# Optimization experiments

Measured on AMD Instinct MI355X. Metric: run time of the kernel, lower is better.

## Reference

```python
import jax, jax.numpy as jnp
import numpy as np

NEG_SLOPE = 0.2  # PyG GATConv default negative_slope


def gat_conv(x, edge_index, W, att_src, att_dst, bias):
    # PyG GATConv, heads=1, add_self_loops=True, lin bias=False, final bias added
    N = x.shape[0]
    h = x @ W                                     # [N, F]
    loops = jnp.arange(N, dtype=edge_index.dtype)
    src = jnp.concatenate([edge_index[0], loops])
    dst = jnp.concatenate([edge_index[1], loops])
    a_src = h @ att_src                           # [N]
    a_dst = h @ att_dst                           # [N]
    e = a_src[src] + a_dst[dst]
    e = jnp.where(e > 0, e, NEG_SLOPE * e)        # leaky_relu
    m = jax.ops.segment_max(e, dst, num_segments=N)
    w = jnp.exp(e - m[dst])
    denom = jax.ops.segment_sum(w, dst, num_segments=N)
    alpha = w / denom[dst]
    out = jax.ops.segment_sum(h[src] * alpha[:, None], dst, num_segments=N)
    return out + bias


def gcn_conv(x, edge_index, W, b):
    # PyG GCNConv: add self-loops + symmetric normalization
    N = x.shape[0]
    loops = jnp.arange(N, dtype=edge_index.dtype)
    src = jnp.concatenate([edge_index[0], loops])
    dst = jnp.concatenate([edge_index[1], loops])
    deg = jax.ops.segment_sum(jnp.ones(src.shape[0], dtype=x.dtype), dst, num_segments=N)
    dinv = jax.lax.rsqrt(jnp.maximum(deg, 1e-12))  # deg >= 1 thanks to self-loops
    norm = dinv[src] * dinv[dst]
    xw = x @ W
    return jax.ops.segment_sum(xw[src] * norm[:, None], dst, num_segments=N) + b


def get_final_node(x, batch, num_graphs):
    nn_ = jax.ops.segment_sum(jnp.ones(x.shape[0], dtype=jnp.int32), batch, num_segments=num_graphs)
    cum = jnp.concatenate([jnp.zeros(1, dtype=nn_.dtype), jnp.cumsum(nn_)[:-1]])
    return x[cum]


def ontology_emb(table, e1, e2, W, asrc, adst, b, idx_map):
    emb = gat_conv(table, e1, W, asrc, adst, b)
    emb = gat_conv(emb, e2, W, asrc, adst, b)
    return emb[idx_map]


def _forward(spec_emb, diag_table, proce_table, atc_table,
             diag_W, diag_asrc, diag_adst, diag_b,
             proce_W, proce_asrc, proce_adst, proce_b,
             atc_W, atc_asrc, atc_adst, atc_b,
             gcn_W1, gcn_b1, gcn_W2, gcn_b2, gcn_W3, gcn_b3,
             diag_e1, diag_e2, proce_e1, proce_e2, atc_e1, atc_e2,
             diag_map, proce_map, atc_map,
             left_x, left_graph_index, right_x, right_graph_index,
             left_x_batch, right_x_batch, num_graphs):
    diag_emb = ontology_emb(diag_table, diag_e1, diag_e2, diag_W, diag_asrc, diag_adst, diag_b, diag_map)
    proce_emb = ontology_emb(proce_table, proce_e1, proce_e2, proce_W, proce_asrc, proce_adst, proce_b, proce_map)
    atc_emb = ontology_emb(atc_table, atc_e1, atc_e2, atc_W, atc_asrc, atc_adst, atc_b, atc_map)
    all_emb = jnp.concatenate([spec_emb, diag_emb, proce_emb, atc_emb], axis=0)
    lh = all_emb[left_x[:, 0]]   # squeeze(dim=1)
    rh = all_emb[right_x[:, 0]]
    for W, b in ((gcn_W1, gcn_b1), (gcn_W2, gcn_b2), (gcn_W3, gcn_b3)):
        lh = gcn_conv(lh, left_graph_index, W, b)
        rh = gcn_conv(rh, right_graph_index, W, b)
    lf = get_final_node(lh, left_x_batch, num_graphs)
    rf = get_final_node(rh, right_x_batch, num_graphs)
    eps = 1e-6  # CosineSimilarity eps
    num = jnp.sum(lf * rf, axis=-1)
    den = jnp.maximum(jnp.linalg.norm(lf, axis=-1), eps) * jnp.maximum(jnp.linalg.norm(rf, axis=-1), eps)
    return num / den


def setup_inputs() -> dict:
    key = jax.random.key(0)
    ks = jax.random.split(key, 32)
    HID = 128
    B, NPG = 2048, 50
    N = B * NPG               # 102400 nodes per side
    E_PAT = 409600            # 4 edges per node
    DIAG_N, DIAG_L = 30000, 20000
    PROCE_N, PROCE_L = 12000, 8000
    ATC_N, ATC_L = 6000, 4000
    ALL = 1 + DIAG_L + PROCE_L + ATC_L
    f = lambda k, s: jax.random.normal(k, s, dtype=jnp.float32)
    scale = 0.1
    inp = {
        'spec_emb': f(ks[0], (1, HID)),
        'diag_table': f(ks[1], (DIAG_N, HID)),
        'proce_table': f(ks[2], (PROCE_N, HID)),
        'atc_table': f(ks[3], (ATC_N, HID)),
    }
    for i, nm in enumerate(['diag', 'proce', 'atc']):
        inp[nm + '_W'] = f(ks[4 + i], (HID, HID)) * scale
        inp[nm + '_asrc'] = f(ks[7 + i], (HID,)) * scale
        inp[nm + '_adst'] = f(ks[10 + i], (HID,)) * scale
        inp[nm + '_b'] = jnp.zeros((HID,), jnp.float32)
    for j in range(3):
        inp['gcn_W%d' % (j + 1)] = f(ks[13 + j], (HID, HID)) * scale
        inp['gcn_b%d' % (j + 1)] = jnp.zeros((HID,), jnp.float32)
    inp['diag_e1'] = jax.random.randint(ks[16], (2, DIAG_N), 0, DIAG_N, dtype=jnp.int32)
    inp['diag_e2'] = jax.random.randint(ks[17], (2, DIAG_N), 0, DIAG_N, dtype=jnp.int32)
    inp['proce_e1'] = jax.random.randint(ks[18], (2, PROCE_N), 0, PROCE_N, dtype=jnp.int32)
    inp['proce_e2'] = jax.random.randint(ks[19], (2, PROCE_N), 0, PROCE_N, dtype=jnp.int32)
    inp['atc_e1'] = jax.random.randint(ks[20], (2, ATC_N), 0, ATC_N, dtype=jnp.int32)
    inp['atc_e2'] = jax.random.randint(ks[21], (2, ATC_N), 0, ATC_N, dtype=jnp.int32)
    inp['diag_map'] = jnp.arange(DIAG_L, dtype=jnp.int32)
    inp['proce_map'] = jnp.arange(PROCE_L, dtype=jnp.int32)
    inp['atc_map'] = jnp.arange(ATC_L, dtype=jnp.int32)
    inp['left_x'] = jax.random.randint(ks[22], (N, 1), 0, ALL, dtype=jnp.int32)
    inp['right_x'] = jax.random.randint(ks[23], (N, 1), 0, ALL, dtype=jnp.int32)
    inp['left_graph_index'] = jax.random.randint(ks[24], (2, E_PAT), 0, N, dtype=jnp.int32)
    inp['right_graph_index'] = jax.random.randint(ks[25], (2, E_PAT), 0, N, dtype=jnp.int32)
    batch = jnp.repeat(jnp.arange(B, dtype=jnp.int32), NPG)
    inp['left_x_batch'] = batch
    inp['right_x_batch'] = batch
    inp['num_graphs'] = B
    return inp


def reference(spec_emb, diag_table, proce_table, atc_table,
              diag_W, diag_asrc, diag_adst, diag_b,
              proce_W, proce_asrc, proce_adst, proce_b,
              atc_W, atc_asrc, atc_adst, atc_b,
              gcn_W1, gcn_b1, gcn_W2, gcn_b2, gcn_W3, gcn_b3,
              diag_e1, diag_e2, proce_e1, proce_e2, atc_e1, atc_e2,
              diag_map, proce_map, atc_map,
              left_x, left_graph_index, right_x, right_graph_index,
              left_x_batch, right_x_batch, num_graphs):
    return _forward(spec_emb, diag_table, proce_table, atc_table,
                    diag_W, diag_asrc, diag_adst, diag_b,
                    proce_W, proce_asrc, proce_adst, proce_b,
                    atc_W, atc_asrc, atc_adst, atc_b,
                    gcn_W1, gcn_b1, gcn_W2, gcn_b2, gcn_W3, gcn_b3,
                    diag_e1, diag_e2, proce_e1, proce_e2, atc_e1, atc_e2,
                    diag_map, proce_map, atc_map,
                    left_x, left_graph_index, right_x, right_graph_index,
                    left_x_batch, right_x_batch, num_graphs)
```

## Files before the change

kernel.cpp:

```cpp
#include <hip/hip_runtime.h>
#include <hip/hip_bf16.h>

#define HID 128

typedef unsigned int uint;
typedef unsigned short ushort;
typedef short short8 __attribute__((ext_vector_type(8)));
typedef float f32x4 __attribute__((ext_vector_type(4)));

static inline int cdiv_i(long a, long b) { return (int)((a + b - 1) / b); }
static inline int imax_i(int a, int b) { return a > b ? a : b; }

__device__ __forceinline__ float bf2f(uint hi) {
    return __builtin_bit_cast(float, hi << 16);
}
__device__ __forceinline__ ushort f2bf(float f) {
    uint u = __builtin_bit_cast(uint, f);
    u = (u + 0x7fffu + ((u >> 16) & 1u)) >> 16;
    return (ushort)u;
}

struct CsrDesc {
    const int* esrc[8];
    const int* edst[8];
    int ebase[9];
    int nbase[9];
    int totE;
};

template <typename AT>
__device__ __forceinline__ void load_afrag(const AT* __restrict__ A, long row,
                                           int koff, short8& af) {
    if constexpr (__is_same(AT, ushort)) {
        const uint4 raw = *(const uint4*)(A + row * 128 + koff);
        af = __builtin_bit_cast(short8, raw);
    } else {
        const float4* p = (const float4*)(A + row * 128 + koff);
        const float4 x0 = p[0], x1 = p[1];
        af[0] = (short)f2bf(x0.x); af[1] = (short)f2bf(x0.y);
        af[2] = (short)f2bf(x0.z); af[3] = (short)f2bf(x0.w);
        af[4] = (short)f2bf(x1.x); af[5] = (short)f2bf(x1.y);
        af[6] = (short)f2bf(x1.z); af[7] = (short)f2bf(x1.w);
    }
}

struct GOnto {
    const ushort* Wt0; const ushort* Wt1; const ushort* Wt2;
    const float* s0; const float* s1; const float* s2;
    const float* d0; const float* d1; const float* d2;
    int bs1, bs2;
    int r1, r2, r3;
};

template <typename AT>
__device__ void gemm_onto_dev(int b, const AT* __restrict__ x0,
                              const AT* __restrict__ x1, const AT* __restrict__ x2,
                              const GOnto& g, ushort* __restrict__ H,
                              float* __restrict__ as_o, float* __restrict__ ad_o) {
    const int gid = (b >= g.bs1) + (b >= g.bs2);
    const ushort* Wt = (gid == 0) ? g.Wt0 : (gid == 1) ? g.Wt1 : g.Wt2;
    const float* avs = (gid == 0) ? g.s0 : (gid == 1) ? g.s1 : g.s2;
    const float* avd = (gid == 0) ? g.d0 : (gid == 1) ? g.d1 : g.d2;
    const AT* Ag = (gid == 0) ? x0 : (gid == 1) ? x1 : x2;
    const int bloc = b - ((gid == 0) ? 0 : (gid == 1) ? g.bs1 : g.bs2);
    const long rb = (gid == 0) ? 0 : (gid == 1) ? g.r1 : g.r2;
    const long Mg = ((gid == 0) ? g.r1 : (gid == 1) ? g.r2 : g.r3) - rb;

    const int tid = threadIdx.x;
    const int wave = tid >> 6, lane = tid & 63;
    const int r = lane & 15, q = lane >> 4;
    const long m0 = (long)bloc * 128 + wave * 32;

    f32x4 acc[2][8];
#pragma unroll
    for (int mi = 0; mi < 2; ++mi)
#pragma unroll
        for (int ni = 0; ni < 8; ++ni) acc[mi][ni] = (f32x4)0.f;

#pragma unroll
    for (int t = 0; t < 4; ++t) {
        const int koff = t * 32 + q * 8;
        short8 bfr[8];
#pragma unroll
        for (int ni = 0; ni < 8; ++ni) {
            const uint4 raw = *(const uint4*)(Wt + (ni * 16 + r) * 128 + koff);
            bfr[ni] = __builtin_bit_cast(short8, raw);
        }
#pragma unroll
        for (int mi = 0; mi < 2; ++mi) {
            long row = m0 + mi * 16 + r;
            if (row >= Mg) row = Mg - 1;
            short8 af;
            load_afrag<AT>(Ag, row, koff, af);
#pragma unroll
            for (int ni = 0; ni < 8; ++ni)
                acc[mi][ni] = __builtin_amdgcn_mfma_f32_16x16x32_bf16(
                    af, bfr[ni], acc[mi][ni], 0, 0, 0);
        }
    }

    ushort* Hg = H + rb * 128;
#pragma unroll
    for (int mi = 0; mi < 2; ++mi) {
#pragma unroll
        for (int ni = 0; ni < 8; ++ni) {
            const int col = ni * 16 + r;
#pragma unroll
            for (int reg = 0; reg < 4; ++reg) {
                const long row = m0 + mi * 16 + q * 4 + reg;
                if (row < Mg) Hg[row * 128 + col] = f2bf(acc[mi][ni][reg]);
            }
        }
    }

    float asv[8], adv[8];
#pragma unroll
    for (int ni = 0; ni < 8; ++ni) {
        asv[ni] = avs[ni * 16 + r];
        adv[ni] = avd[ni * 16 + r];
    }
#pragma unroll
    for (int mi = 0; mi < 2; ++mi) {
#pragma unroll
        for (int reg = 0; reg < 4; ++reg) {
            float ps = 0.f, pd = 0.f;
#pragma unroll
            for (int ni = 0; ni < 8; ++ni) {
                ps += acc[mi][ni][reg] * asv[ni];
                pd += acc[mi][ni][reg] * adv[ni];
            }
#pragma unroll
            for (int o = 1; o < 16; o <<= 1) {
                ps += __shfl_xor(ps, o);
                pd += __shfl_xor(pd, o);
            }
            const long row = m0 + mi * 16 + q * 4 + reg;
            if (r == 0 && row < Mg) {
                as_o[rb + row] = ps;
                ad_o[rb + row] = pd;
            }
        }
    }
}

__global__ __launch_bounds__(256) void gemm_onto_l2(const ushort* __restrict__ x0,
                                                    const ushort* __restrict__ x1,
                                                    const ushort* __restrict__ x2,
                                                    GOnto g, ushort* __restrict__ H,
                                                    float* __restrict__ as_o,
                                                    float* __restrict__ ad_o) {
    gemm_onto_dev<ushort>(blockIdx.x, x0, x1, x2, g, H, as_o, ad_o);
}

struct EmbSrc {
    const float* spec; const ushort* oE;
    const int* m0; const int* m1; const int* m2;
    int lb2, lb3, r1, r2;
};

__device__ __forceinline__ short8 load_emb(const EmbSrc& e, long row, int koff) {
    short8 af;
    if (row == 0) {
        const float4* pp = (const float4*)(e.spec + koff);
        const float4 x0 = pp[0], x1 = pp[1];
        af[0] = (short)f2bf(x0.x); af[1] = (short)f2bf(x0.y);
        af[2] = (short)f2bf(x0.z); af[3] = (short)f2bf(x0.w);
        af[4] = (short)f2bf(x1.x); af[5] = (short)f2bf(x1.y);
        af[6] = (short)f2bf(x1.z); af[7] = (short)f2bf(x1.w);
        return af;
    }
    const int r = (int)row;
    const int seg = (r >= e.lb2) + (r >= e.lb3);
    const int local = r - ((seg == 0) ? 1 : (seg == 1) ? e.lb2 : e.lb3);
    const int* mp = (seg == 0) ? e.m0 : (seg == 1) ? e.m1 : e.m2;
    const int rb = (seg == 0) ? 0 : (seg == 1) ? e.r1 : e.r2;
    const long sr = (long)rb + mp[local];
    return __builtin_bit_cast(short8, *(const uint4*)(e.oE + sr * 128 + koff));
}

__device__ void gemm_pat_tile(const EmbSrc& es, const ushort* __restrict__ Wt,
                              ushort* __restrict__ C, long m0blk, long rowEnd) {
    const int tid = threadIdx.x;
    const int wave = tid >> 6, lane = tid & 63;
    const int r = lane & 15, q = lane >> 4;
    const long m0 = m0blk + wave * 32;

    f32x4 acc[2][8];
#pragma unroll
    for (int mi = 0; mi < 2; ++mi)
#pragma unroll
        for (int ni = 0; ni < 8; ++ni) acc[mi][ni] = (f32x4)0.f;

#pragma unroll
    for (int t = 0; t < 4; ++t) {
        const int koff = t * 32 + q * 8;
        short8 bfr[8];
#pragma unroll
        for (int ni = 0; ni < 8; ++ni) {
            const uint4 raw = *(const uint4*)(Wt + (ni * 16 + r) * 128 + koff);
            bfr[ni] = __builtin_bit_cast(short8, raw);
        }
#pragma unroll
        for (int mi = 0; mi < 2; ++mi) {
            long row = m0 + mi * 16 + r;
            if (row >= rowEnd) row = rowEnd - 1;
            const short8 af = load_emb(es, row, koff);
#pragma unroll
            for (int ni = 0; ni < 8; ++ni)
                acc[mi][ni] = __builtin_amdgcn_mfma_f32_16x16x32_bf16(
                    af, bfr[ni], acc[mi][ni], 0, 0, 0);
        }
    }

#pragma unroll
    for (int mi = 0; mi < 2; ++mi) {
#pragma unroll
        for (int ni = 0; ni < 8; ++ni) {
            const int col = ni * 16 + r;
#pragma unroll
            for (int reg = 0; reg < 4; ++reg) {
                const long row = m0 + mi * 16 + q * 4 + reg;
                if (row < rowEnd) C[row * 128 + col] = f2bf(acc[mi][ni][reg]);
            }
        }
    }
}

__global__ __launch_bounds__(256) void gemm_pat(EmbSrc es,
                                                const ushort* __restrict__ Wt,
                                                ushort* __restrict__ C, int M) {
    const long m0 = (long)blockIdx.x * 256;
    gemm_pat_tile(es, Wt, C, m0, M);
    if (m0 + 128 < M) gemm_pat_tile(es, Wt, C, m0 + 128, M);
}

__device__ __forceinline__ void fold1_dev(int idx, const float* __restrict__ W2,
                                          const float* __restrict__ b2,
                                          const float* __restrict__ W3,
                                          float* __restrict__ W23b) {
    if (idx >= 129 * 128) return;
    const int i = idx >> 7, j = idx & 127;
    const float* a = (i < 128) ? (W2 + i * 128) : b2;
    float s = 0.f;
#pragma unroll 8
    for (int k = 0; k < 128; ++k) s += a[k] * W3[k * 128 + j];
    W23b[idx] = s;
}

__device__ __forceinline__ void fold2_dev(int idx, const float* __restrict__ W1,
                                          const float* __restrict__ b1,
                                          const float* __restrict__ W23b,
                                          ushort* __restrict__ WpT,
                                          float* __restrict__ cbuf) {
    if (idx >= 130 * 128) return;
    const int i = idx >> 7, j = idx & 127;
    if (i == 129) { cbuf[128 + j] = W23b[128 * 128 + j]; return; }
    const float* a = (i < 128) ? (W1 + i * 128) : b1;
    float s = 0.f;
#pragma unroll 8
    for (int k = 0; k < 128; ++k) s += a[k] * W23b[k * 128 + j];
    if (i < 128) WpT[j * 128 + i] = f2bf(s);
    else cbuf[j] = s;
}

__device__ __forceinline__ void mark_dev(int i, const int* __restrict__ lEg,
                                         const int* __restrict__ rEg, int EP,
                                         int NP, int* __restrict__ mk,
                                         int testBit, int setBit) {
    int src, dst;
    if (i < 2 * EP) {
        const int side = i >= EP;
        const int e = i - side * EP;
        const int* eg = side ? rEg : lEg;
        src = side * NP + eg[e];
        dst = side * NP + eg[EP + e];
    } else if (i < 2 * EP + 2 * NP) {
        src = dst = i - 2 * EP;
    } else return;
    if (mk[dst] & testBit) {
        const int old = mk[src];
        if (!(old & setBit)) mk[src] = old | setBit;
    }
}

__device__ __forceinline__ void csr_count_dev(int i, const CsrDesc& d,
                                              int* __restrict__ cnt) {
    if (i >= d.totE) return;
    int li = 0;
#pragma unroll
    for (int k = 1; k < 8; ++k) li += (i >= d.ebase[k]);
    const int v = d.nbase[li] + d.edst[li][i - d.ebase[li]];
    atomicAdd(&cnt[v], 1);
}

struct PackPrep {
    const float* W2; const float* b2; const float* W3; float* W23b;
    const float* wsrc[3]; ushort* wt_out;
    int* cnt; int NV;
    const int* bL; const int* bR; int NP;
    int* gfL; int* gfR; int* mk;
    int nbF1, nbWT, nbInit;
};

__global__ __launch_bounds__(256) void k_prep(PackPrep p) {
    const int b = blockIdx.x, tid = threadIdx.x;
    if (b < p.nbF1) {
        fold1_dev(b * 256 + tid, p.W2, p.b2, p.W3, p.W23b);
    } else if (b < p.nbF1 + p.nbWT) {
        const int idx = (b - p.nbF1) * 256 + tid;
        if (idx < 3 * 16384) {
            const int m = idx >> 14;
            const int e = idx & 16383;
            const int n = e >> 7, k = e & 127;
            p.wt_out[idx] = f2bf(p.wsrc[m][k * 128 + n]);
        }
    } else {
        const int i = (b - p.nbF1 - p.nbWT) * 256 + tid;
        if (i < p.NV) p.cnt[i] = 0;
        if (i < 2 * p.NP) {
            const int side = i >= p.NP;
            const int ii = i - (side ? p.NP : 0);
            const int* bb = side ? p.bR : p.bL;
            int* gf = side ? p.gfR : p.gfL;
            const int cur = bb[ii];
            const int prev = (ii == 0) ? -1 : bb[ii - 1];
            int m = 0;
            if (cur > prev) {
                for (int g = prev + 1; g <= cur; ++g) gf[g] = ii;
                m = 1;
            }
            p.mk[i] = m;
        }
    }
}

struct PackBig {
    const float* x0; const float* x1; const float* x2;
    GOnto go; ushort* H; float* as_o; float* ad_o;
    const float* W1; const float* b1; const float* W23b;
    ushort* WpT; float* cbuf;
    CsrDesc dsc; int* cnt;
    const int* lEg; const int* rEg; int EP; int NP; int* mk;
    int nbGemm, nbF2, nbCnt;
};

__global__ __launch_bounds__(256) void k_big1(PackBig p) {
    const int b = blockIdx.x, tid = threadIdx.x;
    if (b < p.nbGemm) {
        gemm_onto_dev<float>(b, p.x0, p.x1, p.x2, p.go, p.H, p.as_o, p.ad_o);
    } else if (b < p.nbGemm + p.nbF2) {
        fold2_dev((b - p.nbGemm) * 256 + tid, p.W1, p.b1, p.W23b, p.WpT, p.cbuf);
    } else if (b < p.nbGemm + p.nbF2 + p.nbCnt) {
        csr_count_dev((b - p.nbGemm - p.nbF2) * 256 + tid, p.dsc, p.cnt);
    } else {
        mark_dev((b - p.nbGemm - p.nbF2 - p.nbCnt) * 256 + tid, p.lEg, p.rEg,
                 p.EP, p.NP, p.mk, 1, 2);
    }
}

__device__ void scan_tile_dev(const int* __restrict__ in, int* __restrict__ out,
                              int* __restrict__ bsum, int n, int pn0, int pcnt,
                              float* __restrict__ dinv, int tb, int tid,
                              int* sbuf) {
    const int base = tb * 1024 + tid * 4;
    int v[4];
    int s = 0;
#pragma unroll
    for (int k = 0; k < 4; ++k) {
        const int i = base + k;
        v[k] = (i < n) ? (in[i] + 1) : 0;
        if (i >= pn0 && i < pn0 + pcnt)
            dinv[i - pn0] = rsqrtf(fmaxf((float)v[k], 1e-12f));
        s += v[k];
    }
    sbuf[tid] = s;
    __syncthreads();
    int x = s;
    for (int o = 1; o < 256; o <<= 1) {
        const int t = (tid >= o) ? sbuf[tid - o] : 0;
        __syncthreads();
        x += t;
        sbuf[tid] = x;
        __syncthreads();
    }
    int run = x - s;
#pragma unroll
    for (int k = 0; k < 4; ++k) {
        const int i = base + k;
        if (i < n) out[i] = run;
        run += v[k];
    }
    if (tid == 255) bsum[tb] = x;
}

struct PackScan {
    const int* cnt; int* offs; int* bsum;
    int NV; int pn0; int pcnt; float* dinv;
    const int* lEg; const int* rEg; int EP; int NP; int* mk;
    int nbScan;
};

__global__ __launch_bounds__(256) void k_scan(PackScan p) {
    __shared__ int sbuf[256];
    const int b = blockIdx.x, tid = threadIdx.x;
    if (b < p.nbScan) {
        scan_tile_dev(p.cnt, p.offs, p.bsum, p.NV, p.pn0, p.pcnt, p.dinv, b,
                      tid, sbuf);
    } else {
        mark_dev((b - p.nbScan) * 256 + tid, p.lEg, p.rEg, p.EP, p.NP, p.mk,
                 2, 4);
    }
}

__global__ __launch_bounds__(256) void k_scanfin(int* __restrict__ out,
                                                 int* __restrict__ out2,
                                                 const int* __restrict__ bsum,
                                                 int n, int nbData) {
    __shared__ int sbuf[256];
    const int tb = blockIdx.x, tid = threadIdx.x;
    int pLim = tb < nbData ? tb : nbData;
    int pth = 0;
    for (int j = tid; j < pLim; j += 256) pth += bsum[j];
    sbuf[tid] = pth;
    __syncthreads();
    for (int o = 128; o > 0; o >>= 1) {
        if (tid < o) sbuf[tid] += sbuf[tid + o];
        __syncthreads();
    }
    const int prefix = sbuf[0];
    const int base = tb * 1024 + tid * 4;
#pragma unroll
    for (int k = 0; k < 4; ++k) {
        const int i = base + k;
        if (i < n) {
            const int v = out[i] + prefix;
            out[i] = v;
            out2[i] = v;
        } else if (i == n) {
            out[i] = prefix + ((tb < nbData) ? bsum[tb] : 0);
        }
    }
}

struct FillP {
    CsrDesc dsc;
    const int* offs; int* offs2; const int* cnt;
    int* srcl; int4* pedge; const float* dinv;
    const int* lx; const int* rx; const int* mk;
    int NP, pB;
    int eStart, eCount, vStart, vCount;
};

__device__ void fill_dev(const FillP& f, int idx) {
    if (idx < f.eCount) {
        const int i = f.eStart + idx;
        int li = 0;
#pragma unroll
        for (int k = 1; k < 8; ++k) li += (i >= f.dsc.ebase[k]);
        const int j = i - f.dsc.ebase[li];
        const int v = f.dsc.nbase[li] + f.dsc.edst[li][j];
        const int s = f.dsc.esrc[li][j];
        if (li >= 6) {
            const int n2l = v - f.dsc.nbase[6];
            if (f.mk[n2l] == 0) return;
            const int sg = (li - 6) * f.NP + s;
            const int cidx = atomicAdd(&f.offs2[v], 1);
            int4 rec;
            rec.x = sg;
            rec.y = (li == 7 ? f.rx : f.lx)[s];
            rec.z = __float_as_int(f.dinv[n2l] * f.dinv[sg]);
            rec.w = 0;
            f.pedge[cidx - f.pB] = rec;
        } else {
            const int cidx = atomicAdd(&f.offs2[v], 1);
            f.srcl[cidx] = s;
        }
    } else if (idx < f.eCount + f.vCount) {
        const int v = f.vStart + (idx - f.eCount);
        int li = 0;
#pragma unroll
        for (int k = 1; k < 8; ++k) li += (v >= f.dsc.nbase[k]);
        const int s = v - f.dsc.nbase[li];
        if (li >= 6) {
            const int n2l = v - f.dsc.nbase[6];
            if (f.mk[n2l] == 0) return;
            const int cidx = f.offs[v] + f.cnt[v];
            const int sg = (li - 6) * f.NP + s;
            int4 rec;
            rec.x = sg;
            rec.y = (li == 7 ? f.rx : f.lx)[s];
            rec.z = __float_as_int(f.dinv[n2l] * f.dinv[sg]);
            rec.w = 0;
            f.pedge[cidx - f.pB] = rec;
        } else {
            f.srcl[f.offs[v] + f.cnt[v]] = s;
        }
    }
}

__global__ __launch_bounds__(256) void k_fill(FillP f) {
    fill_dev(f, blockIdx.x * 256 + threadIdx.x);
}

struct GatP {
    int r1, r2;
    int ob0, ob1, ob2;
    const float* b0; const float* b1; const float* b2;
};

__device__ __forceinline__ void acc8(float* acc, float w, const uint4 v) {
    acc[0] += w * bf2f(v.x & 0xffff);
    acc[1] += w * bf2f(v.x >> 16);
    acc[2] += w * bf2f(v.y & 0xffff);
    acc[3] += w * bf2f(v.y >> 16);
    acc[4] += w * bf2f(v.z & 0xffff);
    acc[5] += w * bf2f(v.z >> 16);
    acc[6] += w * bf2f(v.w & 0xffff);
    acc[7] += w * bf2f(v.w >> 16);
}

__device__ void gat_dev(int node, int ql, const ushort* __restrict__ h,
                        const float* __restrict__ as, const float* __restrict__ ad,
                        const int* __restrict__ offs, const int* __restrict__ srcl,
                        const GatP& p, ushort* __restrict__ out, int Mtot) {
    if (node >= Mtot) return;
    const int gid = (node >= p.r1) + (node >= p.r2);
    const int rb = (gid == 0) ? 0 : (gid == 1) ? p.r1 : p.r2;
    const int ob = (gid == 0) ? p.ob0 : (gid == 1) ? p.ob1 : p.ob2;
    const float* bias = (gid == 0) ? p.b0 : (gid == 1) ? p.b1 : p.b2;
    const int local = node - rb;
    const int beg = offs[ob + local], end = offs[ob + local + 1];
    const float adv = ad[node];
    float denom = 0.f;
    float acc[8] = {0.f, 0.f, 0.f, 0.f, 0.f, 0.f, 0.f, 0.f};
    int j = beg;
    for (; j + 2 <= end; j += 2) {
        const int s0 = srcl[j], s1 = srcl[j + 1];
        float e0 = as[rb + s0] + adv; e0 = (e0 > 0.f) ? e0 : 0.2f * e0;
        float e1 = as[rb + s1] + adv; e1 = (e1 > 0.f) ? e1 : 0.2f * e1;
        const float w0 = __expf(e0), w1 = __expf(e1);
        const uint4 v0 = *(const uint4*)(h + (size_t)(rb + s0) * 128 + ql * 8);
        const uint4 v1 = *(const uint4*)(h + (size_t)(rb + s1) * 128 + ql * 8);
        denom += w0 + w1;
        acc8(acc, w0, v0);
        acc8(acc, w1, v1);
    }
    if (j < end) {
        const int s0 = srcl[j];
        float e0 = as[rb + s0] + adv; e0 = (e0 > 0.f) ? e0 : 0.2f * e0;
        const float w0 = __expf(e0);
        const uint4 v0 = *(const uint4*)(h + (size_t)(rb + s0) * 128 + ql * 8);
        denom += w0;
        acc8(acc, w0, v0);
    }
    const float inv = 1.f / denom;
    const float4 bv0 = *(const float4*)(bias + ql * 8);
    const float4 bv1 = *(const float4*)(bias + ql * 8 + 4);
    uint4 o;
    o.x = (uint)f2bf(acc[0] * inv + bv0.x) | ((uint)f2bf(acc[1] * inv + bv0.y) << 16);
    o.y = (uint)f2bf(acc[2] * inv + bv0.z) | ((uint)f2bf(acc[3] * inv + bv0.w) << 16);
    o.z = (uint)f2bf(acc[4] * inv + bv1.x) | ((uint)f2bf(acc[5] * inv + bv1.y) << 16);
    o.w = (uint)f2bf(acc[6] * inv + bv1.z) | ((uint)f2bf(acc[7] * inv + bv1.w) << 16);
    *(uint4*)(out + (size_t)node * 128 + ql * 8) = o;
}

__global__ __launch_bounds__(256) void gat_all(const ushort* __restrict__ h,
                                               const float* __restrict__ as,
                                               const float* __restrict__ ad,
                                               const int* __restrict__ offs,
                                               const int* __restrict__ srcl,
                                               GatP p, ushort* __restrict__ out,
                                               int Mtot) {
    gat_dev(blockIdx.x * 16 + (threadIdx.x >> 4), threadIdx.x & 15, h, as, ad,
            offs, srcl, p, out, Mtot);
}

struct GatFill {
    const ushort* h; const float* as; const float* ad;
    const int* offs; const int* srcl;
    GatP gp; ushort* out; int Mtot; int nbGat;
    FillP f;
};

__global__ __launch_bounds__(256) void k_gat_fill(GatFill g) {
    const int b = blockIdx.x, tid = threadIdx.x;
    if (b < g.nbGat) {
        gat_dev(b * 16 + (tid >> 4), tid & 15, g.h, g.as, g.ad, g.offs, g.srcl,
                g.gp, g.out, g.Mtot);
    } else {
        fill_dev(g.f, (b - g.nbGat) * 256 + tid);
    }
}

__global__ __launch_bounds__(256) void gcn_agg1(const ushort* __restrict__ A3,
                                                const int4* __restrict__ pedge,
                                                const int* __restrict__ offs6,
                                                const float* __restrict__ c1,
                                                ushort* __restrict__ t1,
                                                const int* __restrict__ mk,
                                                int NP2, int pB) {
    const int n2 = blockIdx.x * 16 + (threadIdx.x >> 4);
    const int ql = threadIdx.x & 15;
    if (n2 >= NP2) return;
    if ((mk[n2] & 4) == 0) return;
    const int beg = offs6[n2] - pB, end = offs6[n2 + 1] - pB;
    float acc[8] = {0.f, 0.f, 0.f, 0.f, 0.f, 0.f, 0.f, 0.f};
    int j = beg;
    for (; j + 2 <= end; j += 2) {
        const int4 r0 = pedge[j], r1 = pedge[j + 1];
        const float w0 = __int_as_float(r0.z), w1 = __int_as_float(r1.z);
        const uint4 v0 = *(const uint4*)(A3 + (size_t)r0.y * 128 + ql * 8);
        const uint4 v1 = *(const uint4*)(A3 + (size_t)r1.y * 128 + ql * 8);
        acc8(acc, w0, v0);
        acc8(acc, w1, v1);
    }
    if (j < end) {
        const int4 r0 = pedge[j];
        const uint4 v0 = *(const uint4*)(A3 + (size_t)r0.y * 128 + ql * 8);
        acc8(acc, __int_as_float(r0.z), v0);
    }
    const float4 bv0 = *(const float4*)(c1 + ql * 8);
    const float4 bv1 = *(const float4*)(c1 + ql * 8 + 4);
    uint4 o;
    o.x = (uint)f2bf(acc[0] + bv0.x) | ((uint)f2bf(acc[1] + bv0.y) << 16);
    o.y = (uint)f2bf(acc[2] + bv0.z) | ((uint)f2bf(acc[3] + bv0.w) << 16);
    o.z = (uint)f2bf(acc[4] + bv1.x) | ((uint)f2bf(acc[5] + bv1.y) << 16);
    o.w = (uint)f2bf(acc[6] + bv1.z) | ((uint)f2bf(acc[7] + bv1.w) << 16);
    *(uint4*)(t1 + (size_t)n2 * 128 + ql * 8) = o;
}

__device__ __forceinline__ void gcn_q_acc(const ushort* __restrict__ x,
                                          const int4* __restrict__ pedge,
                                          int beg, int end, int ql, float* acc) {
    int j = beg;
    for (; j + 2 <= end; j += 2) {
        const int4 r0 = pedge[j], r1 = pedge[j + 1];
        const float w0 = __int_as_float(r0.z), w1 = __int_as_float(r1.z);
        const uint4 v0 = *(const uint4*)(x + (size_t)r0.x * 128 + ql * 8);
        const uint4 v1 = *(const uint4*)(x + (size_t)r1.x * 128 + ql * 8);
        acc8(acc, w0, v0);
        acc8(acc, w1, v1);
    }
    if (j < end) {
        const int4 r0 = pedge[j];
        const uint4 v0 = *(const uint4*)(x + (size_t)r0.x * 128 + ql * 8);
        acc8(acc, __int_as_float(r0.z), v0);
    }
}

__global__ __launch_bounds__(256) void gcn_agg2(const ushort* __restrict__ t1,
                                                const int4* __restrict__ pedge,
                                                const int* __restrict__ offs6,
                                                const float* __restrict__ c2,
                                                ushort* __restrict__ t2,
                                                const int* __restrict__ mk,
                                                int NP2, int pB) {
    const int n2 = blockIdx.x * 16 + (threadIdx.x >> 4);
    const int ql = threadIdx.x & 15;
    if (n2 >= NP2) return;
    if ((mk[n2] & 2) == 0) return;
    const int beg = offs6[n2] - pB, end = offs6[n2 + 1] - pB;
    float acc[8] = {0.f, 0.f, 0.f, 0.f, 0.f, 0.f, 0.f, 0.f};
    gcn_q_acc(t1, pedge, beg, end, ql, acc);
    const float4 bv0 = *(const float4*)(c2 + ql * 8);
    const float4 bv1 = *(const float4*)(c2 + ql * 8 + 4);
    uint4 o;
    o.x = (uint)f2bf(acc[0] + bv0.x) | ((uint)f2bf(acc[1] + bv0.y) << 16);
    o.y = (uint)f2bf(acc[2] + bv0.z) | ((uint)f2bf(acc[3] + bv0.w) << 16);
    o.z = (uint)f2bf(acc[4] + bv1.x) | ((uint)f2bf(acc[5] + bv1.y) << 16);
    o.w = (uint)f2bf(acc[6] + bv1.z) | ((uint)f2bf(acc[7] + bv1.w) << 16);
    *(uint4*)(t2 + (size_t)n2 * 128 + ql * 8) = o;
}

__global__ __launch_bounds__(256) void final_cos(const ushort* __restrict__ t2,
                                                 const int4* __restrict__ pedge,
                                                 const int* __restrict__ offs6,
                                                 const int* __restrict__ gfL,
                                                 const int* __restrict__ gfR,
                                                 const float* __restrict__ b3,
                                                 float* __restrict__ out,
                                                 int B, int NP, int pB) {
    const int g = blockIdx.x * 8 + (threadIdx.x >> 5);
    const int l32 = threadIdx.x & 31;
    const int side = l32 >> 4;
    const int ql = l32 & 15;
    if (g >= B) return;
    const int n2 = (side ? NP : 0) + (side ? gfR : gfL)[g];
    const int beg = offs6[n2] - pB, end = offs6[n2 + 1] - pB;
    float acc[8] = {0.f, 0.f, 0.f, 0.f, 0.f, 0.f, 0.f, 0.f};
    gcn_q_acc(t2, pedge, beg, end, ql, acc);
    const float4 bv0 = *(const float4*)(b3 + ql * 8);
    const float4 bv1 = *(const float4*)(b3 + ql * 8 + 4);
    float v[8];
    v[0] = acc[0] + bv0.x; v[1] = acc[1] + bv0.y;
    v[2] = acc[2] + bv0.z; v[3] = acc[3] + bv0.w;
    v[4] = acc[4] + bv1.x; v[5] = acc[5] + bv1.y;
    v[6] = acc[6] + bv1.z; v[7] = acc[7] + bv1.w;
    float num = 0.f, nself = 0.f, nother = 0.f;
#pragma unroll
    for (int j = 0; j < 8; ++j) {
        const float o = __shfl_xor(v[j], 16);
        num += v[j] * o;
        nself += v[j] * v[j];
        nother += o * o;
    }
#pragma unroll
    for (int o1 = 1; o1 < 16; o1 <<= 1) {
        num += __shfl_xor(num, o1);
        nself += __shfl_xor(nself, o1);
        nother += __shfl_xor(nother, o1);
    }
    if (l32 == 0)
        out[g] = num / (fmaxf(sqrtf(nself), 1e-6f) * fmaxf(sqrtf(nother), 1e-6f));
}

extern "C" void kernel_launch(void* const* d_in, const int* in_sizes, int n_in,
                              void* d_out, int out_size, void* d_ws, size_t ws_size,
                              hipStream_t stream) {
    (void)n_in; (void)ws_size;
    const float* spec = (const float*)d_in[0];
    const float* tabs[3] = {(const float*)d_in[1], (const float*)d_in[2], (const float*)d_in[3]};
    const float* ontW[3] = {(const float*)d_in[4], (const float*)d_in[8], (const float*)d_in[12]};
    const float* ontAs[3] = {(const float*)d_in[5], (const float*)d_in[9], (const float*)d_in[13]};
    const float* ontAd[3] = {(const float*)d_in[6], (const float*)d_in[10], (const float*)d_in[14]};
    const float* ontB[3] = {(const float*)d_in[7], (const float*)d_in[11], (const float*)d_in[15]};
    const float* gcnW[3] = {(const float*)d_in[16], (const float*)d_in[18], (const float*)d_in[20]};
    const float* gcnB[3] = {(const float*)d_in[17], (const float*)d_in[19], (const float*)d_in[21]};
    const int* e1s[3] = {(const int*)d_in[22], (const int*)d_in[24], (const int*)d_in[26]};
    const int* e2s[3] = {(const int*)d_in[23], (const int*)d_in[25], (const int*)d_in[27]};
    const int* maps[3] = {(const int*)d_in[28], (const int*)d_in[29], (const int*)d_in[30]};
    const int* left_x = (const int*)d_in[31];
    const int* right_x = (const int*)d_in[32];
    const int* left_eg = (const int*)d_in[33];
    const int* right_eg = (const int*)d_in[34];
    const int* left_batch = (const int*)d_in[35];
    const int* right_batch = (const int*)d_in[36];

    int Ms[3] = {in_sizes[1] / HID, in_sizes[2] / HID, in_sizes[3] / HID};
    int E1s[3] = {in_sizes[22] / 2, in_sizes[24] / 2, in_sizes[26] / 2};
    int E2s[3] = {in_sizes[23] / 2, in_sizes[25] / 2, in_sizes[27] / 2};
    int Ls[3] = {in_sizes[28], in_sizes[29], in_sizes[30]};
    const int NP = in_sizes[31];
    const int EP = in_sizes[33] / 2;
    const int B = out_size;
    const long ALL = 1 + (long)Ls[0] + Ls[1] + Ls[2];
    const int Mtot = Ms[0] + Ms[1] + Ms[2];
    const int r1 = Ms[0], r2 = Ms[0] + Ms[1];

    CsrDesc dsc;
    int eCnt[8], nCnt[8];
    for (int i = 0; i < 3; ++i) {
        dsc.esrc[i] = e1s[i];     dsc.edst[i] = e1s[i] + E1s[i];
        eCnt[i] = E1s[i];         nCnt[i] = Ms[i];
        dsc.esrc[3 + i] = e2s[i]; dsc.edst[3 + i] = e2s[i] + E2s[i];
        eCnt[3 + i] = E2s[i];     nCnt[3 + i] = Ms[i];
    }
    dsc.esrc[6] = left_eg;  dsc.edst[6] = left_eg + EP;  eCnt[6] = EP; nCnt[6] = NP;
    dsc.esrc[7] = right_eg; dsc.edst[7] = right_eg + EP; eCnt[7] = EP; nCnt[7] = NP;
    dsc.ebase[0] = 0;
    int nb_acc = 0;
    for (int i = 0; i < 8; ++i) {
        dsc.ebase[i + 1] = dsc.ebase[i] + eCnt[i];
        dsc.nbase[i] = nb_acc;
        nb_acc += nCnt[i];
    }
    const int NV = nb_acc;
    dsc.nbase[8] = NV;
    dsc.totE = dsc.ebase[8];
    const int totEntries = dsc.totE + NV;
    const int pB = dsc.ebase[6] + dsc.nbase[6];
    const int pEntries = totEntries - pB;

    char* ws = (char*)d_ws;
    size_t off = 0;
    auto alloc = [&](size_t bytes) -> void* {
        off = (off + 255) & ~(size_t)255;
        void* p = ws + off;
        off += bytes;
        return p;
    };
    ushort* wt4 = (ushort*)alloc((size_t)4 * 16384 * 2);
    float* W23b = (float*)alloc((size_t)129 * 128 * 4);
    float* cbuf = (float*)alloc((size_t)256 * 4);
    ushort* A3 = (ushort*)alloc((size_t)ALL * HID * 2);
    int* cnt = (int*)alloc((size_t)NV * 4);
    int* offs = (int*)alloc((size_t)(NV + 1) * 4);
    int* offs2 = (int*)alloc((size_t)NV * 4);
    int* srcl = (int*)alloc((size_t)pB * 4);
    int4* pedge = (int4*)alloc((size_t)pEntries * 16);
    int* bsum = (int*)alloc(1025 * 4);
    float* dinv = (float*)alloc((size_t)2 * NP * 4);
    float* as = (float*)alloc((size_t)Mtot * 4);
    float* ad = (float*)alloc((size_t)Mtot * 4);
    int* gfL = (int*)alloc((size_t)(B + 1) * 4);
    int* gfR = (int*)alloc((size_t)(B + 1) * 4);
    int* mk = (int*)alloc((size_t)2 * NP * 4);
    ushort* t1 = (ushort*)alloc((size_t)2 * NP * HID * 2);
    ushort* big = (ushort*)alloc((size_t)2 * NP * HID * 2);
    ushort* hbuf = big;
    ushort* obuf = big + (size_t)Mtot * HID;
    ushort* t2 = big;

    const ushort* wtOnt[3] = {wt4, wt4 + 16384, wt4 + 2 * 16384};
    ushort* WpT = wt4 + 3 * 16384;
    const float* c1 = cbuf;
    const float* c2 = cbuf + 128;

    PackPrep pp;
    pp.W2 = gcnW[1]; pp.b2 = gcnB[1]; pp.W3 = gcnW[2]; pp.W23b = W23b;
    pp.wsrc[0] = ontW[0]; pp.wsrc[1] = ontW[1]; pp.wsrc[2] = ontW[2];
    pp.wt_out = wt4;
    pp.cnt = cnt; pp.NV = NV;
    pp.bL = left_batch; pp.bR = right_batch; pp.NP = NP;
    pp.gfL = gfL; pp.gfR = gfR; pp.mk = mk;
    pp.nbF1 = cdiv_i(129 * 128, 256);
    pp.nbWT = cdiv_i(3 * 16384, 256);
    pp.nbInit = cdiv_i(imax_i(NV, 2 * NP), 256);
    k_prep<<<pp.nbF1 + pp.nbWT + pp.nbInit, 256, 0, stream>>>(pp);

    GOnto go;
    go.Wt0 = wtOnt[0]; go.Wt1 = wtOnt[1]; go.Wt2 = wtOnt[2];
    go.s0 = ontAs[0]; go.s1 = ontAs[1]; go.s2 = ontAs[2];
    go.d0 = ontAd[0]; go.d1 = ontAd[1]; go.d2 = ontAd[2];
    go.bs1 = cdiv_i(Ms[0], 128);
    go.bs2 = go.bs1 + cdiv_i(Ms[1], 128);
    const int totBlk = go.bs2 + cdiv_i(Ms[2], 128);
    go.r1 = r1; go.r2 = r2; go.r3 = Mtot;

    PackBig pg;
    pg.x0 = tabs[0]; pg.x1 = tabs[1]; pg.x2 = tabs[2];
    pg.go = go; pg.H = hbuf; pg.as_o = as; pg.ad_o = ad;
    pg.W1 = gcnW[0]; pg.b1 = gcnB[0]; pg.W23b = W23b;
    pg.WpT = WpT; pg.cbuf = cbuf;
    pg.dsc = dsc; pg.cnt = cnt;
    pg.lEg = left_eg; pg.rEg = right_eg; pg.EP = EP; pg.NP = NP; pg.mk = mk;
    pg.nbGemm = totBlk;
    pg.nbF2 = cdiv_i(130 * 128, 256);
    pg.nbCnt = cdiv_i(dsc.totE, 256);
    const int nbMark = cdiv_i(2 * EP + 2 * NP, 256);
    k_big1<<<pg.nbGemm + pg.nbF2 + pg.nbCnt + nbMark, 256, 0, stream>>>(pg);

    PackScan psn;
    psn.cnt = cnt; psn.offs = offs; psn.bsum = bsum;
    psn.NV = NV; psn.pn0 = dsc.nbase[6]; psn.pcnt = 2 * NP; psn.dinv = dinv;
    psn.lEg = left_eg; psn.rEg = right_eg; psn.EP = EP; psn.NP = NP; psn.mk = mk;
    psn.nbScan = cdiv_i(NV, 1024);
    k_scan<<<psn.nbScan + nbMark, 256, 0, stream>>>(psn);

    k_scanfin<<<cdiv_i(NV + 1, 1024), 256, 0, stream>>>(offs, offs2, bsum, NV,
                                                        psn.nbScan);

    FillP fb;
    fb.dsc = dsc; fb.offs = offs; fb.offs2 = offs2; fb.cnt = cnt;
    fb.srcl = srcl; fb.pedge = pedge; fb.dinv = dinv;
    fb.lx = left_x; fb.rx = right_x; fb.mk = mk;
    fb.NP = NP; fb.pB = pB;

    FillP fo = fb;
    fo.eStart = 0;             fo.eCount = dsc.ebase[3];
    fo.vStart = 0;             fo.vCount = dsc.nbase[3];
    k_fill<<<cdiv_i(fo.eCount + fo.vCount, 256), 256, 0, stream>>>(fo);

    GatFill gf;
    gf.h = hbuf; gf.as = as; gf.ad = ad; gf.offs = offs; gf.srcl = srcl;
    gf.gp = GatP{r1, r2, dsc.nbase[0], dsc.nbase[1], dsc.nbase[2],
                 ontB[0], ontB[1], ontB[2]};
    gf.out = obuf; gf.Mtot = Mtot;
    gf.nbGat = cdiv_i(Mtot, 16);
    gf.f = fb;
    gf.f.eStart = dsc.ebase[3]; gf.f.eCount = dsc.totE - dsc.ebase[3];
    gf.f.vStart = dsc.nbase[3]; gf.f.vCount = NV - dsc.nbase[3];
    k_gat_fill<<<gf.nbGat + cdiv_i(gf.f.eCount + gf.f.vCount, 256), 256, 0,
                 stream>>>(gf);

    gemm_onto_l2<<<totBlk, 256, 0, stream>>>(obuf, obuf + (size_t)r1 * HID,
                                             obuf + (size_t)r2 * HID, go, hbuf,
                                             as, ad);
    const GatP gp1{r1, r2, dsc.nbase[3], dsc.nbase[4], dsc.nbase[5],
                   ontB[0], ontB[1], ontB[2]};
    gat_all<<<cdiv_i(Mtot, 16), 256, 0, stream>>>(hbuf, as, ad, offs, srcl, gp1,
                                                  obuf, Mtot);

    EmbSrc es;
    es.spec = spec; es.oE = obuf;
    es.m0 = maps[0]; es.m1 = maps[1]; es.m2 = maps[2];
    es.lb2 = 1 + Ls[0]; es.lb3 = 1 + Ls[0] + Ls[1];
    es.r1 = r1; es.r2 = r2;
    gemm_pat<<<cdiv_i(ALL, 256), 256, 0, stream>>>(es, WpT, A3, (int)ALL);

    const int* offs6 = offs + dsc.nbase[6];
    gcn_agg1<<<cdiv_i(2 * NP, 16), 256, 0, stream>>>(A3, pedge, offs6, c1, t1,
                                                     mk, 2 * NP, pB);
    gcn_agg2<<<cdiv_i(2 * NP, 16), 256, 0, stream>>>(t1, pedge, offs6, c2, t2,
                                                     mk, 2 * NP, pB);
    final_cos<<<cdiv_i(B, 8), 256, 0, stream>>>(t2, pedge, offs6, gfL, gfR,
                                                gcnB[2], (float*)d_out, B, NP, pB);
}
```

Measured before the change: 334.3 us.

## Pack CSR degree counters into bytes and shrink GEMM tiles to 64 rows

Replaces the per-node int degree counters with 8-bit fields packed four to a uint. Counting uses shifted atomicAdds and the scan and fill kernels read the counters through byte extraction. This shrinks the counter memory and lets the scan read one word per thread, but it assumes no in-degree exceeds 255. Separately, the ontology and pattern GEMMs now use 64-row blocks with one 16-row MFMA tile per wave, giving more blocks and fewer registers but re-reading the B fragments more often.

```diff
diff --git a/kernel.cpp b/kernel.cpp
--- a/kernel.cpp
+++ b/kernel.cpp
@@ -18,6 +18,10 @@
     uint u = __builtin_bit_cast(uint, f);
     u = (u + 0x7fffu + ((u >> 16) & 1u)) >> 16;
     return (ushort)u;
+}
+
+__device__ __forceinline__ int cnt_rd(const uint* __restrict__ cnt, int v) {
+    return (int)((cnt[v >> 2] >> ((v & 3) * 8)) & 0xffu);
 }
 
 struct CsrDesc {
@@ -69,13 +73,11 @@
     const int tid = threadIdx.x;
     const int wave = tid >> 6, lane = tid & 63;
     const int r = lane & 15, q = lane >> 4;
-    const long m0 = (long)bloc * 128 + wave * 32;
-
-    f32x4 acc[2][8];
-#pragma unroll
-    for (int mi = 0; mi < 2; ++mi)
-#pragma unroll
-        for (int ni = 0; ni < 8; ++ni) acc[mi][ni] = (f32x4)0.f;
+    const long m0 = (long)bloc * 64 + wave * 16;
+
+    f32x4 acc[8];
+#pragma unroll
+    for (int ni = 0; ni < 8; ++ni) acc[ni] = (f32x4)0.f;
 
 #pragma unroll
     for (int t = 0; t < 4; ++t) {
@@ -86,30 +88,24 @@
             const uint4 raw = *(const uint4*)(Wt + (ni * 16 + r) * 128 + koff);
             bfr[ni] = __builtin_bit_cast(short8, raw);
         }
-#pragma unroll
-        for (int mi = 0; mi < 2; ++mi) {
-            long row = m0 + mi * 16 + r;
-            if (row >= Mg) row = Mg - 1;
-            short8 af;
-            load_afrag<AT>(Ag, row, koff, af);
-#pragma unroll
-            for (int ni = 0; ni < 8; ++ni)
-                acc[mi][ni] = __builtin_amdgcn_mfma_f32_16x16x32_bf16(
-                    af, bfr[ni], acc[mi][ni], 0, 0, 0);
-        }
+        long row = m0 + r;
+        if (row >= Mg) row = Mg - 1;
+        short8 af;
+        load_afrag<AT>(Ag, row, koff, af);
+#pragma unroll
+        for (int ni = 0; ni < 8; ++ni)
+            acc[ni] = __builtin_amdgcn_mfma_f32_16x16x32_bf16(af, bfr[ni],
+                                                              acc[ni], 0, 0, 0);
     }
 
     ushort* Hg = H + rb * 128;
 #pragma unroll
-    for (int mi = 0; mi < 2; ++mi) {
-#pragma unroll
-        for (int ni = 0; ni < 8; ++ni) {
-            const int col = ni * 16 + r;
-#pragma unroll
-            for (int reg = 0; reg < 4; ++reg) {
-                const long row = m0 + mi * 16 + q * 4 + reg;
-                if (row < Mg) Hg[row * 128 + col] = f2bf(acc[mi][ni][reg]);
-            }
+    for (int ni = 0; ni < 8; ++ni) {
+        const int col = ni * 16 + r;
+#pragma unroll
+        for (int reg = 0; reg < 4; ++reg) {
+            const long row = m0 + q * 4 + reg;
+            if (row < Mg) Hg[row * 128 + col] = f2bf(acc[ni][reg]);
         }
     }
 
@@ -120,25 +116,22 @@
         adv[ni] = avd[ni * 16 + r];
     }
 #pragma unroll
-    for (int mi = 0; mi < 2; ++mi) {
-#pragma unroll
-        for (int reg = 0; reg < 4; ++reg) {
-            float ps = 0.f, pd = 0.f;
-#pragma unroll
-            for (int ni = 0; ni < 8; ++ni) {
-                ps += acc[mi][ni][reg] * asv[ni];
-                pd += acc[mi][ni][reg] * adv[ni];
-            }
-#pragma unroll
-            for (int o = 1; o < 16; o <<= 1) {
-                ps += __shfl_xor(ps, o);
-                pd += __shfl_xor(pd, o);
-            }
-            const long row = m0 + mi * 16 + q * 4 + reg;
-            if (r == 0 && row < Mg) {
-                as_o[rb + row] = ps;
-                ad_o[rb + row] = pd;
-            }
+    for (int reg = 0; reg < 4; ++reg) {
+        float ps = 0.f, pd = 0.f;
+#pragma unroll
+        for (int ni = 0; ni < 8; ++ni) {
+            ps += acc[ni][reg] * asv[ni];
+            pd += acc[ni][reg] * adv[ni];
+        }
+#pragma unroll
+        for (int o = 1; o < 16; o <<= 1) {
+            ps += __shfl_xor(ps, o);
+            pd += __shfl_xor(pd, o);
+        }
+        const long row = m0 + q * 4 + reg;
+        if (r == 0 && row < Mg) {
+            as_o[rb + row] = ps;
+            ad_o[rb + row] = pd;
         }
     }
 }
@@ -178,18 +171,17 @@
     return __builtin_bit_cast(short8, *(const uint4*)(e.oE + sr * 128 + koff));
 }
 
-__device__ void gemm_pat_tile(const EmbSrc& es, const ushort* __restrict__ Wt,
-                              ushort* __restrict__ C, long m0blk, long rowEnd) {
+__global__ __launch_bounds__(256) void gemm_pat(EmbSrc es,
+                                                const ushort* __restrict__ Wt,
+                                                ushort* __restrict__ C, int M) {
     const int tid = threadIdx.x;
     const int wave = tid >> 6, lane = tid & 63;
     const int r = lane & 15, q = lane >> 4;
-    const long m0 = m0blk + wave * 32;
-
-    f32x4 acc[2][8];
-#pragma unroll
-    for (int mi = 0; mi < 2; ++mi)
-#pragma unroll
-        for (int ni = 0; ni < 8; ++ni) acc[mi][ni] = (f32x4)0.f;
+    const long m0 = (long)blockIdx.x * 64 + wave * 16;
+
+    f32x4 acc[8];
+#pragma unroll
+    for (int ni = 0; ni < 8; ++ni) acc[ni] = (f32x4)0.f;
 
 #pragma unroll
     for (int t = 0; t < 4; ++t) {
@@ -200,38 +192,24 @@
             const uint4 raw = *(const uint4*)(Wt + (ni * 16 + r) * 128 + koff);
             bfr[ni] = __builtin_bit_cast(short8, raw);
         }
-#pragma unroll
-        for (int mi = 0; mi < 2; ++mi) {
-            long row = m0 + mi * 16 + r;
-            if (row >= rowEnd) row = rowEnd - 1;
-            const short8 af = load_emb(es, row, koff);
-#pragma unroll
-            for (int ni = 0; ni < 8; ++ni)
-                acc[mi][ni] = __builtin_amdgcn_mfma_f32_16x16x32_bf16(
-                    af, bfr[ni], acc[mi][ni], 0, 0, 0);
-        }
-    }
-
-#pragma unroll
-    for (int mi = 0; mi < 2; ++mi) {
-#pragma unroll
-        for (int ni = 0; ni < 8; ++ni) {
-            const int col = ni * 16 + r;
-#pragma unroll
-            for (int reg = 0; reg < 4; ++reg) {
-                const long row = m0 + mi * 16 + q * 4 + reg;
-                if (row < rowEnd) C[row * 128 + col] = f2bf(acc[mi][ni][reg]);
-            }
-        }
-    }
-}
-
-__global__ __launch_bounds__(256) void gemm_pat(EmbSrc es,
-                                                const ushort* __restrict__ Wt,
-                                                ushort* __restrict__ C, int M) {
-    const long m0 = (long)blockIdx.x * 256;
-    gemm_pat_tile(es, Wt, C, m0, M);
-    if (m0 + 128 < M) gemm_pat_tile(es, Wt, C, m0 + 128, M);
+        long row = m0 + r;
+        if (row >= M) row = M - 1;
+        const short8 af = load_emb(es, row, koff);
+#pragma unroll
+        for (int ni = 0; ni < 8; ++ni)
+            acc[ni] = __builtin_amdgcn_mfma_f32_16x16x32_bf16(af, bfr[ni],
+                                                              acc[ni], 0, 0, 0);
+    }
+
+#pragma unroll
+    for (int ni = 0; ni < 8; ++ni) {
+        const int col = ni * 16 + r;
+#pragma unroll
+        for (int reg = 0; reg < 4; ++reg) {
+            const long row = m0 + q * 4 + reg;
+            if (row < M) C[row * 128 + col] = f2bf(acc[ni][reg]);
+        }
+    }
 }
 
 __device__ __forceinline__ void fold1_dev(int idx, const float* __restrict__ W2,
@@ -284,19 +262,19 @@
 }
 
 __device__ __forceinline__ void csr_count_dev(int i, const CsrDesc& d,
-                                              int* __restrict__ cnt) {
+                                              uint* __restrict__ cnt) {
     if (i >= d.totE) return;
     int li = 0;
 #pragma unroll
     for (int k = 1; k < 8; ++k) li += (i >= d.ebase[k]);
     const int v = d.nbase[li] + d.edst[li][i - d.ebase[li]];
-    atomicAdd(&cnt[v], 1);
+    atomicAdd(&cnt[v >> 2], 1u << ((v & 3) * 8));
 }
 
 struct PackPrep {
     const float* W2; const float* b2; const float* W3; float* W23b;
     const float* wsrc[3]; ushort* wt_out;
-    int* cnt; int NV;
+    uint* cnt; int cntW;
     const int* bL; const int* bR; int NP;
     int* gfL; int* gfR; int* mk;
     int nbF1, nbWT, nbInit;
@@ -316,7 +294,7 @@
         }
     } else {
         const int i = (b - p.nbF1 - p.nbWT) * 256 + tid;
-        if (i < p.NV) p.cnt[i] = 0;
+        if (i < p.cntW) p.cnt[i] = 0;
         if (i < 2 * p.NP) {
             const int side = i >= p.NP;
             const int ii = i - (side ? p.NP : 0);
@@ -339,7 +317,7 @@
     GOnto go; ushort* H; float* as_o; float* ad_o;
     const float* W1; const float* b1; const float* W23b;
     ushort* WpT; float* cbuf;
-    CsrDesc dsc; int* cnt;
+    CsrDesc dsc; uint* cnt;
     const int* lEg; const int* rEg; int EP; int NP; int* mk;
     int nbGemm, nbF2, nbCnt;
 };
@@ -358,17 +336,18 @@
     }
 }
 
-__device__ void scan_tile_dev(const int* __restrict__ in, int* __restrict__ out,
+__device__ void scan_tile_dev(const uint* __restrict__ in, int* __restrict__ out,
                               int* __restrict__ bsum, int n, int pn0, int pcnt,
                               float* __restrict__ dinv, int tb, int tid,
                               int* sbuf) {
     const int base = tb * 1024 + tid * 4;
+    const uint word = in[tb * 256 + tid];
     int v[4];
     int s = 0;
 #pragma unroll
     for (int k = 0; k < 4; ++k) {
         const int i = base + k;
-        v[k] = (i < n) ? (in[i] + 1) : 0;
+        v[k] = (i < n) ? (int)((word >> (k * 8)) & 0xffu) + 1 : 0;
         if (i >= pn0 && i < pn0 + pcnt)
             dinv[i - pn0] = rsqrtf(fmaxf((float)v[k], 1e-12f));
         s += v[k];
@@ -394,7 +373,7 @@
 }
 
 struct PackScan {
-    const int* cnt; int* offs; int* bsum;
+    const uint* cnt; int* offs; int* bsum;
     int NV; int pn0; int pcnt; float* dinv;
     const int* lEg; const int* rEg; int EP; int NP; int* mk;
     int nbScan;
@@ -444,7 +423,7 @@
 
 struct FillP {
     CsrDesc dsc;
-    const int* offs; int* offs2; const int* cnt;
+    const int* offs; int* offs2; const uint* cnt;
     int* srcl; int4* pedge; const float* dinv;
     const int* lx; const int* rx; const int* mk;
     int NP, pB;
@@ -484,7 +463,7 @@
         if (li >= 6) {
             const int n2l = v - f.dsc.nbase[6];
             if (f.mk[n2l] == 0) return;
-            const int cidx = f.offs[v] + f.cnt[v];
+            const int cidx = f.offs[v] + cnt_rd(f.cnt, v);
             const int sg = (li - 6) * f.NP + s;
             int4 rec;
             rec.x = sg;
@@ -493,7 +472,7 @@
             rec.w = 0;
             f.pedge[cidx - f.pB] = rec;
         } else {
-            f.srcl[f.offs[v] + f.cnt[v]] = s;
+            f.srcl[f.offs[v] + cnt_rd(f.cnt, v)] = s;
         }
     }
 }
@@ -770,6 +749,7 @@
     const int totEntries = dsc.totE + NV;
     const int pB = dsc.ebase[6] + dsc.nbase[6];
     const int pEntries = totEntries - pB;
+    const int cntW = cdiv_i(NV, 4) + 1;
 
     char* ws = (char*)d_ws;
     size_t off = 0;
@@ -783,7 +763,7 @@
     float* W23b = (float*)alloc((size_t)129 * 128 * 4);
     float* cbuf = (float*)alloc((size_t)256 * 4);
     ushort* A3 = (ushort*)alloc((size_t)ALL * HID * 2);
-    int* cnt = (int*)alloc((size_t)NV * 4);
+    uint* cnt = (uint*)alloc((size_t)cntW * 4);
     int* offs = (int*)alloc((size_t)(NV + 1) * 4);
     int* offs2 = (int*)alloc((size_t)NV * 4);
     int* srcl = (int*)alloc((size_t)pB * 4);
@@ -810,21 +790,21 @@
     pp.W2 = gcnW[1]; pp.b2 = gcnB[1]; pp.W3 = gcnW[2]; pp.W23b = W23b;
     pp.wsrc[0] = ontW[0]; pp.wsrc[1] = ontW[1]; pp.wsrc[2] = ontW[2];
     pp.wt_out = wt4;
-    pp.cnt = cnt; pp.NV = NV;
+    pp.cnt = cnt; pp.cntW = cntW;
     pp.bL = left_batch; pp.bR = right_batch; pp.NP = NP;
     pp.gfL = gfL; pp.gfR = gfR; pp.mk = mk;
     pp.nbF1 = cdiv_i(129 * 128, 256);
     pp.nbWT = cdiv_i(3 * 16384, 256);
-    pp.nbInit = cdiv_i(imax_i(NV, 2 * NP), 256);
+    pp.nbInit = cdiv_i(imax_i(cntW, 2 * NP), 256);
     k_prep<<<pp.nbF1 + pp.nbWT + pp.nbInit, 256, 0, stream>>>(pp);
 
     GOnto go;
     go.Wt0 = wtOnt[0]; go.Wt1 = wtOnt[1]; go.Wt2 = wtOnt[2];
     go.s0 = ontAs[0]; go.s1 = ontAs[1]; go.s2 = ontAs[2];
     go.d0 = ontAd[0]; go.d1 = ontAd[1]; go.d2 = ontAd[2];
-    go.bs1 = cdiv_i(Ms[0], 128);
-    go.bs2 = go.bs1 + cdiv_i(Ms[1], 128);
-    const int totBlk = go.bs2 + cdiv_i(Ms[2], 128);
+    go.bs1 = cdiv_i(Ms[0], 64);
+    go.bs2 = go.bs1 + cdiv_i(Ms[1], 64);
+    const int totBlk = go.bs2 + cdiv_i(Ms[2], 64);
     go.r1 = r1; go.r2 = r2; go.r3 = Mtot;
 
     PackBig pg;
@@ -886,7 +866,7 @@
     es.m0 = maps[0]; es.m1 = maps[1]; es.m2 = maps[2];
     es.lb2 = 1 + Ls[0]; es.lb3 = 1 + Ls[0] + Ls[1];
     es.r1 = r1; es.r2 = r2;
-    gemm_pat<<<cdiv_i(ALL, 256), 256, 0, stream>>>(es, WpT, A3, (int)ALL);
+    gemm_pat<<<cdiv_i(ALL, 64), 256, 0, stream>>>(es, WpT, A3, (int)ALL);
 
     const int* offs6 = offs + dsc.nbase[6];
     gcn_agg1<<<cdiv_i(2 * NP, 16), 256, 0, stream>>>(A3, pedge, offs6, c1, t1,
```

Result: slower. 345.6 us (+3.4%).
